# Performance work log

Measured on AMD Instinct MI355X. Metric: run time of the kernel, lower is better.

The kernel has to match this reference:

```python
import jax, jax.numpy as jnp
import numpy as np

B, S, SK = 4, 1024, 1024
Q_IN, KV_IN = 1024, 1024
G, DQ, DV = 16, 64, 64
OUT = Q_IN
EPS = 1e-5


def setup_inputs() -> dict:
    key = jax.random.key(0)
    ks = jax.random.split(key, 12)
    s_q = 1.0 / np.sqrt(Q_IN)
    s_kv = 1.0 / np.sqrt(KV_IN)
    s_p = 1.0 / np.sqrt(G * DV)
    return {
        "Q": jax.random.normal(ks[0], (B, S, Q_IN), jnp.float32),
        "KV": jax.random.normal(ks[1], (B, SK, KV_IN), jnp.float32),
        "Wq": jax.random.normal(ks[2], (G * DQ, Q_IN), jnp.float32) * s_q,
        "bq": jax.random.normal(ks[3], (G * DQ,), jnp.float32) * s_q,
        "Wk": jax.random.normal(ks[4], (G * DQ, KV_IN), jnp.float32) * s_kv,
        "bk": jax.random.normal(ks[5], (G * DQ,), jnp.float32) * s_kv,
        "Wv": jax.random.normal(ks[6], (G * DV, KV_IN), jnp.float32) * s_kv,
        "bv": jax.random.normal(ks[7], (G * DV,), jnp.float32) * s_kv,
        "Wp": jax.random.normal(ks[8], (OUT, G * DV), jnp.float32) * s_p,
        "bp": jax.random.normal(ks[9], (OUT,), jnp.float32) * s_p,
        "gamma": jnp.ones((OUT,), jnp.float32),
        "beta": jnp.zeros((OUT,), jnp.float32),
    }


def reference(Q, KV, Wq, bq, Wk, bk, Wv, bv, Wp, bp, gamma, beta):
    b, s, _ = Q.shape
    sk = KV.shape[1]
    inv_sqrt_dim = DQ ** (-0.5)

    # projections
    q = Q @ Wq.T + bq            # [b, s, G*DQ]
    k = KV @ Wk.T + bk           # [b, sk, G*DQ]
    v = KV @ Wv.T + bv           # [b, sk, G*DV]

    # q/k: group is the SLOW axis; v: group is the FAST axis (faithful to source)
    q = q.reshape(b, s, G, DQ)               # [b, s, g, d]
    k = k.reshape(b, sk, G, DQ)              # [b, sk, g, d]
    v = v.reshape(b, sk, DV, G)              # [b, sk, d, g]

    logits = jnp.einsum('bsgd,btgd->bgst', q, k) * inv_sqrt_dim  # [b, g, s, sk]
    scores = jax.nn.softmax(logits, axis=-1)
    attn = jnp.einsum('bgst,btdg->bgsd', scores, v)              # [b, g, s, dv]

    # flatten as (dv, g): feature index = d*G + g  (faithful to source permute)
    attn = attn.transpose(0, 2, 3, 1).reshape(b, s, DV * G)
    out = attn @ Wp.T + bp + Q

    # LayerNorm
    mu = out.mean(axis=-1, keepdims=True)
    var = out.var(axis=-1, keepdims=True)
    out = (out - mu) * jax.lax.rsqrt(var + EPS) * gamma + beta

    return out, scores.reshape(b * G, s, sk)
```

## Files before the change

kernel.cpp:

```cpp
#include <hip/hip_runtime.h>

typedef __attribute__((ext_vector_type(8))) short short8;
typedef __attribute__((ext_vector_type(4))) short s16x4;
typedef __attribute__((ext_vector_type(4))) float f32x4;

static __device__ __forceinline__ short f2bf(float x) {
  union { float f; unsigned u; } v; v.f = x;
  unsigned r = (v.u + 0x7fffu + ((v.u >> 16) & 1u)) >> 16;
  return (short)r;
}
static __device__ __forceinline__ float bf2f(short x) {
  union { unsigned u; float f; } v; v.u = ((unsigned)(unsigned short)x) << 16;
  return v.f;
}

static __device__ __forceinline__ void gld16(const short* g, short* l) {
  __builtin_amdgcn_global_load_lds(
      (const __attribute__((address_space(1))) unsigned*)g,
      (__attribute__((address_space(3))) unsigned*)l, 16, 0, 0);
}

static __device__ __forceinline__ void conv8(const float* __restrict__ src,
                                             short* __restrict__ dst, int i,
                                             float scale) {
  const f32x4* s = (const f32x4*)(src + (long)i * 8);
  f32x4 a = s[0], b = s[1];
  short8 o;
  o[0] = f2bf(a[0] * scale); o[1] = f2bf(a[1] * scale);
  o[2] = f2bf(a[2] * scale); o[3] = f2bf(a[3] * scale);
  o[4] = f2bf(b[0] * scale); o[5] = f2bf(b[1] * scale);
  o[6] = f2bf(b[2] * scale); o[7] = f2bf(b[3] * scale);
  *(short8*)(dst + (long)i * 8) = o;
}

__global__ __launch_bounds__(256) void prep(
    const float* __restrict__ Q, const float* __restrict__ KV,
    const float* __restrict__ Wq, const float* __restrict__ Wk,
    const float* __restrict__ Wv, const float* __restrict__ Wp,
    const float* __restrict__ bq,
    short* __restrict__ Qb, short* __restrict__ KVb,
    short* __restrict__ Wqb, short* __restrict__ Wkb,
    short* __restrict__ Wvb, short* __restrict__ Wpb,
    float* __restrict__ bqs) {
  const int blk = blockIdx.x, tid = threadIdx.x;
  if (blk < 2048) {
    conv8(Q, Qb, blk * 256 + tid, 1.f);
  } else if (blk < 4096) {
    conv8(KV, KVb, (blk - 2048) * 256 + tid, 1.f);
  } else if (blk < 4608) {
    conv8(Wq, Wqb, (blk - 4096) * 256 + tid, 0.125f);
  } else if (blk < 5120) {
    conv8(Wk, Wkb, (blk - 4608) * 256 + tid, 1.f);
  } else if (blk < 5632) {
    conv8(Wv, Wvb, (blk - 5120) * 256 + tid, 1.f);
  } else if (blk < 6656) {
    __shared__ float row[1024];
    const long o = blk - 5632;
    *(f32x4*)&row[tid * 4] = *(const f32x4*)(Wp + o * 1024 + tid * 4);
    __syncthreads();
    const int f0 = tid * 4;
    s16x4 t;
#pragma unroll
    for (int j = 0; j < 4; ++j) {
      int f = f0 + j;
      t[j] = f2bf(row[((f & 63) << 4) + (f >> 6)]);
    }
    *(s16x4*)(Wpb + o * 1024 + f0) = t;
  } else {
    int i = (blk - 6656) * 256 + tid;
    bqs[i] = bq[i] * 0.125f;
  }
}

template <typename OutT>
static __device__ __forceinline__ void gemm_core(
    const short* __restrict__ A, const short* __restrict__ B,
    OutT* __restrict__ C, const float* __restrict__ bias,
    const float* __restrict__ resid, int bm, int bn, int omode,
    short (*As)[128 * 64], short (*Bs)[128 * 64]) {
  const int tid = threadIdx.x, lane = tid & 63, wave = tid >> 6;
  const int fr = lane & 15, khi = lane >> 4;
  const int wr = wave >> 1, wc = wave & 1;

  f32x4 acc[4][4];
#pragma unroll
  for (int m = 0; m < 4; ++m)
#pragma unroll
    for (int n = 0; n < 4; ++n) acc[m][n] = (f32x4){0.f, 0.f, 0.f, 0.f};

  auto stage = [&](int buf, int k0) {
#pragma unroll
    for (int it = 0; it < 4; ++it) {
      int l = it * 256 + tid;
      int r = l >> 3, c = (l & 7) ^ (r & 7);
      gld16(A + (long)(bm + r) * 1024 + k0 + c * 8, &As[buf][l * 8]);
      gld16(B + (long)(bn + r) * 1024 + k0 + c * 8, &Bs[buf][l * 8]);
    }
  };

  stage(0, 0);
  __syncthreads();
  int cur = 0;
  for (int k0 = 0; k0 < 1024; k0 += 64) {
    if (k0 < 960) stage(cur ^ 1, k0 + 64);
#pragma unroll
    for (int ks = 0; ks < 64; ks += 32) {
      const int cc = (ks >> 3) + khi;
      short8 af[4], bf[4];
#pragma unroll
      for (int m = 0; m < 4; ++m) {
        const int ar = wr * 64 + m * 16 + fr;
        af[m] = *(const short8*)&As[cur][ar * 64 + ((cc ^ (ar & 7)) * 8)];
      }
#pragma unroll
      for (int n = 0; n < 4; ++n) {
        const int br = wc * 64 + n * 16 + fr;
        bf[n] = *(const short8*)&Bs[cur][br * 64 + ((cc ^ (br & 7)) * 8)];
      }
#pragma unroll
      for (int m = 0; m < 4; ++m)
#pragma unroll
        for (int n = 0; n < 4; ++n)
          acc[m][n] = __builtin_amdgcn_mfma_f32_16x16x32_bf16(af[m], bf[n],
                                                              acc[m][n], 0, 0, 0);
    }
    __syncthreads();
    cur ^= 1;
  }

  const int col0 = lane & 15, row0 = (lane >> 4) * 4;
#pragma unroll
  for (int m = 0; m < 4; ++m) {
#pragma unroll
    for (int n = 0; n < 4; ++n) {
      const int gcol = bn + wc * 64 + n * 16 + col0;
      const float bi = bias[gcol];
#pragma unroll
      for (int i = 0; i < 4; ++i) {
        const int grow = bm + wr * 64 + m * 16 + row0 + i;
        float v = acc[m][n][i] + bi;
        if (resid) v += resid[(long)grow * 1024 + gcol];
        long addr;
        if (omode == 0)
          addr = (long)grow * 1024 + gcol;
        else
          addr = ((long)(grow >> 10) << 20) + ((long)gcol << 10) + (grow & 1023);
        if constexpr (sizeof(OutT) == 2)
          C[addr] = (OutT)f2bf(v);
        else
          C[addr] = v;
      }
    }
  }
}

__global__ __launch_bounds__(256, 2) void proj_all(
    const short* __restrict__ Qb, const short* __restrict__ KVb,
    const short* __restrict__ Wqb, const short* __restrict__ Wkb,
    const short* __restrict__ Wvb,
    const float* __restrict__ bqs, const float* __restrict__ bk,
    const float* __restrict__ bv,
    short* __restrict__ qb, short* __restrict__ kb, short* __restrict__ vt) {
  __shared__ short As[2][128 * 64];
  __shared__ short Bs[2][128 * 64];
  int bid = blockIdx.x;
  int swz = (bid & 7) * 96 + (bid >> 3);
  const int seg = swz >> 8, local = swz & 255;
  const int bm = (local >> 3) * 128, bn = (local & 7) * 128;
  if (seg == 0)
    gemm_core<short>(Qb, Wqb, qb, bqs, nullptr, bm, bn, 0, As, Bs);
  else if (seg == 1)
    gemm_core<short>(KVb, Wkb, kb, bk, nullptr, bm, bn, 0, As, Bs);
  else
    gemm_core<short>(KVb, Wvb, vt, bv, nullptr, bm, bn, 1, As, Bs);
}

__global__ __launch_bounds__(256, 2) void out_gemm(
    const short* __restrict__ at, const short* __restrict__ Wpb,
    const float* __restrict__ bp, const float* __restrict__ Q,
    float* __restrict__ pre) {
  __shared__ short As[2][128 * 64];
  __shared__ short Bs[2][128 * 64];
  int bid = blockIdx.x;
  int swz = (bid & 7) * 32 + (bid >> 3);
  const int bm = (swz >> 3) * 128, bn = (swz & 7) * 128;
  gemm_core<float>(at, Wpb, pre, bp, Q, bm, bn, 0, As, Bs);
}

__global__ __launch_bounds__(256, 3) void fused_attn(
    const short* __restrict__ qb,
    const short* __restrict__ kb,
    const short* __restrict__ vt,
    float* __restrict__ scores,
    short* __restrict__ at) {
  constexpr int LP = 72;
  __shared__ short Ks[2][64 * 64];
  __shared__ short Vs[2][64 * 64];
  __shared__ short Ps[128 * LP];

  int bid = blockIdx.x;
  bid = (bid & 7) * 64 + (bid >> 3);
  const int z = bid >> 3, b = z >> 4, g = z & 15;
  const int q0 = (bid & 7) * 128;

  const int tid = threadIdx.x, lane = tid & 63, w = tid >> 6;
  const int fr = lane & 15, khi = lane >> 4;
  const long bqk = (long)b << 20;
  const int qr = q0 + w * 32;

  short8 aq[4];
#pragma unroll
  for (int sub = 0; sub < 2; ++sub) {
    const short* qrow = qb + bqk + (long)(qr + sub * 16 + fr) * 1024 + g * 64 + khi * 8;
    aq[sub * 2] = *(const short8*)qrow;
    aq[sub * 2 + 1] = *(const short8*)(qrow + 32);
  }
  const short* kgp = kb + bqk + g * 64;
  const short* vgp = vt + bqk;

  auto stageK = [&](int buf, int t0) {
#pragma unroll
    for (int it = 0; it < 2; ++it) {
      int l = it * 256 + tid;
      int r = l >> 3, c = (l & 7) ^ (r & 7);
      gld16(kgp + (long)(t0 + r) * 1024 + c * 8, &Ks[buf][l * 8]);
    }
  };
  auto stageV = [&](int buf, int t0) {
#pragma unroll
    for (int it = 0; it < 2; ++it) {
      int l = it * 256 + tid;
      int r = l >> 3, c = (l & 7) ^ (r & 7);
      gld16(vgp + ((long)(r * 16 + g) << 10) + t0 + c * 8, &Vs[buf][l * 8]);
    }
  };

  float s4[2][4] = {{0.f, 0.f, 0.f, 0.f}, {0.f, 0.f, 0.f, 0.f}};
  stageK(0, 0);
  __syncthreads();
  int cur = 0;
  for (int t0 = 0; t0 < 1024; t0 += 64) {
    if (t0 < 960) stageK(cur ^ 1, t0 + 64);
#pragma unroll
    for (int nf = 0; nf < 4; ++nf) {
      const int r2 = nf * 16 + fr;
      short8 b0 = *(const short8*)&Ks[cur][r2 * 64 + (khi ^ (r2 & 7)) * 8];
      short8 b1 = *(const short8*)&Ks[cur][r2 * 64 + ((khi + 4) ^ (r2 & 7)) * 8];
#pragma unroll
      for (int sub = 0; sub < 2; ++sub) {
        f32x4 sacc = (f32x4){0.f, 0.f, 0.f, 0.f};
        sacc = __builtin_amdgcn_mfma_f32_16x16x32_bf16(aq[sub * 2], b0, sacc, 0, 0, 0);
        sacc = __builtin_amdgcn_mfma_f32_16x16x32_bf16(aq[sub * 2 + 1], b1, sacc, 0, 0, 0);
#pragma unroll
        for (int i = 0; i < 4; ++i) s4[sub][i] += __expf(sacc[i]);
      }
    }
    __syncthreads();
    cur ^= 1;
  }
  float inv4[2][4];
#pragma unroll
  for (int sub = 0; sub < 2; ++sub)
#pragma unroll
    for (int i = 0; i < 4; ++i) {
      float s = s4[sub][i];
      s += __shfl_xor(s, 1);
      s += __shfl_xor(s, 2);
      s += __shfl_xor(s, 4);
      s += __shfl_xor(s, 8);
      inv4[sub][i] = 1.f / s;
    }

  f32x4 pacc[2][4];
#pragma unroll
  for (int sub = 0; sub < 2; ++sub)
#pragma unroll
    for (int nv = 0; nv < 4; ++nv) pacc[sub][nv] = (f32x4){0.f, 0.f, 0.f, 0.f};

  stageK(0, 0);
  stageV(0, 0);
  __syncthreads();
  cur = 0;
  for (int t0 = 0; t0 < 1024; t0 += 64) {
    if (t0 < 960) {
      stageK(cur ^ 1, t0 + 64);
      stageV(cur ^ 1, t0 + 64);
    }
#pragma unroll
    for (int nf = 0; nf < 4; ++nf) {
      const int r2 = nf * 16 + fr;
      short8 b0 = *(const short8*)&Ks[cur][r2 * 64 + (khi ^ (r2 & 7)) * 8];
      short8 b1 = *(const short8*)&Ks[cur][r2 * 64 + ((khi + 4) ^ (r2 & 7)) * 8];
#pragma unroll
      for (int sub = 0; sub < 2; ++sub) {
        f32x4 sacc = (f32x4){0.f, 0.f, 0.f, 0.f};
        sacc = __builtin_amdgcn_mfma_f32_16x16x32_bf16(aq[sub * 2], b0, sacc, 0, 0, 0);
        sacc = __builtin_amdgcn_mfma_f32_16x16x32_bf16(aq[sub * 2 + 1], b1, sacc, 0, 0, 0);
#pragma unroll
        for (int i = 0; i < 4; ++i)
          Ps[(w * 32 + sub * 16 + khi * 4 + i) * LP + nf * 16 + fr] =
              f2bf(__expf(sacc[i]) * inv4[sub][i]);
      }
    }

#pragma unroll
    for (int ks = 0; ks < 64; ks += 32) {
      const int cc = (ks >> 3) + khi;
      short8 ap[2];
#pragma unroll
      for (int sub = 0; sub < 2; ++sub)
        ap[sub] = *(const short8*)&Ps[(w * 32 + sub * 16 + fr) * LP + ks + khi * 8];
#pragma unroll
      for (int nv = 0; nv < 4; ++nv) {
        const int dr = nv * 16 + fr;
        short8 bvv = *(const short8*)&Vs[cur][dr * 64 + (cc ^ (dr & 7)) * 8];
#pragma unroll
        for (int sub = 0; sub < 2; ++sub)
          pacc[sub][nv] =
              __builtin_amdgcn_mfma_f32_16x16x32_bf16(ap[sub], bvv, pacc[sub][nv], 0, 0, 0);
      }
    }

#pragma unroll
    for (int ri = 0; ri < 8; ++ri) {
      const int row = ri * 4 + khi;
      s16x4 pv4 = *(const s16x4*)&Ps[(w * 32 + row) * LP + fr * 4];
      f32x4 o;
      o[0] = bf2f(pv4[0]); o[1] = bf2f(pv4[1]);
      o[2] = bf2f(pv4[2]); o[3] = bf2f(pv4[3]);
      __builtin_nontemporal_store(
          o, (f32x4*)&scores[((long)z << 20) + ((long)(qr + row) << 10) + t0 + fr * 4]);
    }
    __syncthreads();
    cur ^= 1;
  }

#pragma unroll
  for (int sub = 0; sub < 2; ++sub)
#pragma unroll
    for (int nv = 0; nv < 4; ++nv)
#pragma unroll
      for (int i = 0; i < 4; ++i)
        at[bqk + ((long)(qr + sub * 16 + khi * 4 + i) << 10) + g * 64 + nv * 16 + fr] =
            f2bf(pacc[sub][nv][i]);
}

__global__ __launch_bounds__(256) void layernorm_rows(const float* __restrict__ X,
                                                      const float* __restrict__ gamma,
                                                      const float* __restrict__ beta,
                                                      float* __restrict__ O) {
  const int row = blockIdx.x * 4 + (threadIdx.x >> 6);
  const int lane = threadIdx.x & 63;
  const float* x = X + (long)row * 1024 + lane * 4;
  f32x4 v[4];
  float s = 0.f, sq = 0.f;
#pragma unroll
  for (int j = 0; j < 4; ++j) {
    v[j] = *(const f32x4*)(x + j * 256);
#pragma unroll
    for (int e = 0; e < 4; ++e) {
      s += v[j][e];
      sq += v[j][e] * v[j][e];
    }
  }
#pragma unroll
  for (int off = 32; off; off >>= 1) {
    s += __shfl_xor(s, off);
    sq += __shfl_xor(sq, off);
  }
  const float mu = s * (1.f / 1024.f);
  const float var = sq * (1.f / 1024.f) - mu * mu;
  const float rstd = rsqrtf(var + 1e-5f);
  float* o = O + (long)row * 1024 + lane * 4;
#pragma unroll
  for (int j = 0; j < 4; ++j) {
    f32x4 g = *(const f32x4*)(gamma + lane * 4 + j * 256);
    f32x4 be = *(const f32x4*)(beta + lane * 4 + j * 256);
    f32x4 r;
#pragma unroll
    for (int e = 0; e < 4; ++e) r[e] = (v[j][e] - mu) * rstd * g[e] + be[e];
    *(f32x4*)(o + j * 256) = r;
  }
}

extern "C" void kernel_launch(void* const* d_in, const int* in_sizes, int n_in,
                              void* d_out, int out_size, void* d_ws, size_t ws_size,
                              hipStream_t stream) {
  const float* Q = (const float*)d_in[0];
  const float* KV = (const float*)d_in[1];
  const float* Wq = (const float*)d_in[2];
  const float* bq = (const float*)d_in[3];
  const float* Wk = (const float*)d_in[4];
  const float* bk = (const float*)d_in[5];
  const float* Wv = (const float*)d_in[6];
  const float* bv = (const float*)d_in[7];
  const float* Wp = (const float*)d_in[8];
  const float* bp = (const float*)d_in[9];
  const float* gamma = (const float*)d_in[10];
  const float* beta = (const float*)d_in[11];

  float* out = (float*)d_out;
  float* scores = out + (long)4 * 1024 * 1024;

  char* ws = (char*)d_ws;
  short* Wqb = (short*)(ws);
  short* Wkb = (short*)(ws + (2L << 20));
  short* Wvb = (short*)(ws + (4L << 20));
  short* Wpb = (short*)(ws + (6L << 20));
  short* qb  = (short*)(ws + (8L << 20));
  short* kb  = (short*)(ws + (16L << 20));
  short* vt  = (short*)(ws + (24L << 20));
  short* at  = (short*)(ws + (32L << 20));
  float* pre = (float*)(ws + (40L << 20));
  short* Qb  = (short*)(ws + (40L << 20));
  short* KVb = (short*)(ws + (48L << 20));
  float* bqs = (float*)(ws + (56L << 20));
  (void)ws_size; (void)in_sizes; (void)n_in; (void)out_size;

  prep<<<6660, 256, 0, stream>>>(Q, KV, Wq, Wk, Wv, Wp, bq,
                                 Qb, KVb, Wqb, Wkb, Wvb, Wpb, bqs);

  proj_all<<<768, 256, 0, stream>>>(Qb, KVb, Wqb, Wkb, Wvb, bqs, bk, bv,
                                    qb, kb, vt);

  fused_attn<<<512, 256, 0, stream>>>(qb, kb, vt, scores, at);

  out_gemm<<<256, 256, 0, stream>>>(at, Wpb, bp, Q, pre);

  layernorm_rows<<<1024, 256, 0, stream>>>(pre, gamma, beta, out);
}
```

Before: 178.3 us.

## Permute K tile columns so scores are written directly from MFMA registers

Remaps which K rows each lane's MFMA output column covers (r2 = fr*4+nf) and changes the K staging swizzle to match. Each lane now owns four contiguous score columns and stores fp32 scores straight from registers, replacing the LDS round-trip read-back with its bf16 to fp32 reconversion. P is packed into LDS with v_cvt_pk_bf16_f32 in 8-byte stores. Scores are written in fp32 before bf16 rounding, so they differ slightly from the old bf16-rounded values. More accumulator registers are live at once.

Result: no change. 175.6 us (-1.5%).

```diff
diff --git a/kernel.cpp b/kernel.cpp
--- a/kernel.cpp
+++ b/kernel.cpp
@@ -3,15 +3,17 @@
 typedef __attribute__((ext_vector_type(8))) short short8;
 typedef __attribute__((ext_vector_type(4))) short s16x4;
 typedef __attribute__((ext_vector_type(4))) float f32x4;
+typedef __attribute__((ext_vector_type(2))) unsigned u32x2;
 
 static __device__ __forceinline__ short f2bf(float x) {
   union { float f; unsigned u; } v; v.f = x;
   unsigned r = (v.u + 0x7fffu + ((v.u >> 16) & 1u)) >> 16;
   return (short)r;
 }
-static __device__ __forceinline__ float bf2f(short x) {
-  union { unsigned u; float f; } v; v.u = ((unsigned)(unsigned short)x) << 16;
-  return v.f;
+static __device__ __forceinline__ unsigned cvtpk(float lo, float hi) {
+  unsigned r;
+  asm("v_cvt_pk_bf16_f32 %0, %1, %2" : "=v"(r) : "v"(lo), "v"(hi));
+  return r;
 }
 
 static __device__ __forceinline__ void gld16(const short* g, short* l) {
@@ -222,7 +224,7 @@
 #pragma unroll
     for (int it = 0; it < 2; ++it) {
       int l = it * 256 + tid;
-      int r = l >> 3, c = (l & 7) ^ (r & 7);
+      int r = l >> 3, c = (l & 7) ^ ((l >> 5) & 7);
       gld16(kgp + (long)(t0 + r) * 1024 + c * 8, &Ks[buf][l * 8]);
     }
   };
@@ -234,6 +236,8 @@
       gld16(vgp + ((long)(r * 16 + g) << 10) + t0 + c * 8, &Vs[buf][l * 8]);
     }
   };
+
+  const int xk = fr & 7;
 
   float s4[2][4] = {{0.f, 0.f, 0.f, 0.f}, {0.f, 0.f, 0.f, 0.f}};
   stageK(0, 0);
@@ -241,20 +245,30 @@
   int cur = 0;
   for (int t0 = 0; t0 < 1024; t0 += 64) {
     if (t0 < 960) stageK(cur ^ 1, t0 + 64);
+    f32x4 sacc[2][4];
+#pragma unroll
+    for (int sub = 0; sub < 2; ++sub)
+#pragma unroll
+      for (int nf = 0; nf < 4; ++nf) sacc[sub][nf] = (f32x4){0.f, 0.f, 0.f, 0.f};
 #pragma unroll
     for (int nf = 0; nf < 4; ++nf) {
-      const int r2 = nf * 16 + fr;
-      short8 b0 = *(const short8*)&Ks[cur][r2 * 64 + (khi ^ (r2 & 7)) * 8];
-      short8 b1 = *(const short8*)&Ks[cur][r2 * 64 + ((khi + 4) ^ (r2 & 7)) * 8];
+      const int r2 = fr * 4 + nf;
+      short8 b0 = *(const short8*)&Ks[cur][r2 * 64 + ((khi ^ xk) * 8)];
+      short8 b1 = *(const short8*)&Ks[cur][r2 * 64 + (((khi + 4) ^ xk) * 8)];
 #pragma unroll
       for (int sub = 0; sub < 2; ++sub) {
-        f32x4 sacc = (f32x4){0.f, 0.f, 0.f, 0.f};
-        sacc = __builtin_amdgcn_mfma_f32_16x16x32_bf16(aq[sub * 2], b0, sacc, 0, 0, 0);
-        sacc = __builtin_amdgcn_mfma_f32_16x16x32_bf16(aq[sub * 2 + 1], b1, sacc, 0, 0, 0);
-#pragma unroll
-        for (int i = 0; i < 4; ++i) s4[sub][i] += __expf(sacc[i]);
-      }
-    }
+        sacc[sub][nf] =
+            __builtin_amdgcn_mfma_f32_16x16x32_bf16(aq[sub * 2], b0, sacc[sub][nf], 0, 0, 0);
+        sacc[sub][nf] =
+            __builtin_amdgcn_mfma_f32_16x16x32_bf16(aq[sub * 2 + 1], b1, sacc[sub][nf], 0, 0, 0);
+      }
+    }
+#pragma unroll
+    for (int sub = 0; sub < 2; ++sub)
+#pragma unroll
+      for (int nf = 0; nf < 4; ++nf)
+#pragma unroll
+        for (int i = 0; i < 4; ++i) s4[sub][i] += __expf(sacc[sub][nf][i]);
     __syncthreads();
     cur ^= 1;
   }
@@ -286,20 +300,39 @@
       stageK(cur ^ 1, t0 + 64);
       stageV(cur ^ 1, t0 + 64);
     }
+    f32x4 sacc[2][4];
+#pragma unroll
+    for (int sub = 0; sub < 2; ++sub)
+#pragma unroll
+      for (int nf = 0; nf < 4; ++nf) sacc[sub][nf] = (f32x4){0.f, 0.f, 0.f, 0.f};
 #pragma unroll
     for (int nf = 0; nf < 4; ++nf) {
-      const int r2 = nf * 16 + fr;
-      short8 b0 = *(const short8*)&Ks[cur][r2 * 64 + (khi ^ (r2 & 7)) * 8];
-      short8 b1 = *(const short8*)&Ks[cur][r2 * 64 + ((khi + 4) ^ (r2 & 7)) * 8];
+      const int r2 = fr * 4 + nf;
+      short8 b0 = *(const short8*)&Ks[cur][r2 * 64 + ((khi ^ xk) * 8)];
+      short8 b1 = *(const short8*)&Ks[cur][r2 * 64 + (((khi + 4) ^ xk) * 8)];
 #pragma unroll
       for (int sub = 0; sub < 2; ++sub) {
-        f32x4 sacc = (f32x4){0.f, 0.f, 0.f, 0.f};
-        sacc = __builtin_amdgcn_mfma_f32_16x16x32_bf16(aq[sub * 2], b0, sacc, 0, 0, 0);
-        sacc = __builtin_amdgcn_mfma_f32_16x16x32_bf16(aq[sub * 2 + 1], b1, sacc, 0, 0, 0);
-#pragma unroll
-        for (int i = 0; i < 4; ++i)
-          Ps[(w * 32 + sub * 16 + khi * 4 + i) * LP + nf * 16 + fr] =
-              f2bf(__expf(sacc[i]) * inv4[sub][i]);
+        sacc[sub][nf] =
+            __builtin_amdgcn_mfma_f32_16x16x32_bf16(aq[sub * 2], b0, sacc[sub][nf], 0, 0, 0);
+        sacc[sub][nf] =
+            __builtin_amdgcn_mfma_f32_16x16x32_bf16(aq[sub * 2 + 1], b1, sacc[sub][nf], 0, 0, 0);
+      }
+    }
+#pragma unroll
+    for (int sub = 0; sub < 2; ++sub) {
+#pragma unroll
+      for (int i = 0; i < 4; ++i) {
+        f32x4 o;
+#pragma unroll
+        for (int nf = 0; nf < 4; ++nf)
+          o[nf] = __expf(sacc[sub][nf][i]) * inv4[sub][i];
+        const int row = sub * 16 + khi * 4 + i;
+        __builtin_nontemporal_store(
+            o, (f32x4*)&scores[((long)z << 20) + ((long)(qr + row) << 10) + t0 + fr * 4]);
+        u32x2 pp;
+        pp[0] = cvtpk(o[0], o[1]);
+        pp[1] = cvtpk(o[2], o[3]);
+        *(u32x2*)&Ps[(w * 32 + row) * LP + fr * 4] = pp;
       }
     }
 
@@ -313,23 +346,12 @@
 #pragma unroll
       for (int nv = 0; nv < 4; ++nv) {
         const int dr = nv * 16 + fr;
-        short8 bvv = *(const short8*)&Vs[cur][dr * 64 + (cc ^ (dr & 7)) * 8];
+        short8 bvv = *(const short8*)&Vs[cur][dr * 64 + ((cc ^ (dr & 7)) * 8)];
 #pragma unroll
         for (int sub = 0; sub < 2; ++sub)
           pacc[sub][nv] =
               __builtin_amdgcn_mfma_f32_16x16x32_bf16(ap[sub], bvv, pacc[sub][nv], 0, 0, 0);
       }
-    }
-
-#pragma unroll
-    for (int ri = 0; ri < 8; ++ri) {
-      const int row = ri * 4 + khi;
-      s16x4 pv4 = *(const s16x4*)&Ps[(w * 32 + row) * LP + fr * 4];
-      f32x4 o;
-      o[0] = bf2f(pv4[0]); o[1] = bf2f(pv4[1]);
-      o[2] = bf2f(pv4[2]); o[3] = bf2f(pv4[3]);
-      __builtin_nontemporal_store(
-          o, (f32x4*)&scores[((long)z << 20) + ((long)(qr + row) << 10) + t0 + fr * 4]);
     }
     __syncthreads();
     cur ^= 1;
```
